# Optimization experiments

Measured on AMD Instinct MI355X. Metric: run time of the kernel, lower is better.

Reference implementation:

```python
import jax, jax.numpy as jnp
import numpy as np

B, S, E, NUM_CLASSES = 4, 4096, 256, 16

def setup_inputs() -> dict:
    key = jax.random.key(0)
    ks = jax.random.split(key, 10)
    std = E ** -0.5
    return {
        "x":  jax.random.normal(ks[0], (B, S, E), dtype=jnp.float32),
        "wq": jax.random.normal(ks[1], (E, E), dtype=jnp.float32) * std,
        "bq": jnp.zeros((E,), dtype=jnp.float32),
        "wk": jax.random.normal(ks[2], (E, E), dtype=jnp.float32) * std,
        "bk": jnp.zeros((E,), dtype=jnp.float32),
        "wv": jax.random.normal(ks[3], (E, E), dtype=jnp.float32) * std,
        "bv": jnp.zeros((E,), dtype=jnp.float32),
        "wo": jax.random.normal(ks[4], (NUM_CLASSES, E), dtype=jnp.float32) * std,
        "bo": jnp.zeros((NUM_CLASSES,), dtype=jnp.float32),
    }

def reference(x, wq, bq, wk, bk, wv, bv, wo, bo):
    embed_dim = wq.shape[0]
    scaling = embed_dim ** -0.5  # float(embed_dim) ** (-0.5)
    # torch Linear: y = x @ W.T + b
    Q = jnp.einsum('bse,oe->bso', x, wq) + bq
    K = jnp.einsum('bse,oe->bso', x, wk) + bk
    V = jnp.einsum('bse,oe->bso', x, wv) + bv
    # scores: [B, S, S]
    scores = jnp.einsum('bqe,bke->bqk', Q, K) * scaling
    # original code has `/ (embed_dim ^ 0.5)`; intended math is / sqrt(embed_dim)
    attn = jax.nn.softmax(scores, axis=-1) * scaling
    attn_out = jnp.einsum('bqk,bke->bqe', attn, V)
    return jnp.einsum('bqe,oe->bqo', attn_out, wo) + bo
```

## Files before the change

kernel.cpp:

```cpp
#include <hip/hip_runtime.h>
#include <hip/hip_bf16.h>


#define S_ 4096
#define E_ 256
#define B_ 4
#define NC_ 16
#define BS_ (B_ * S_)
#define NS_ 4

typedef __attribute__((ext_vector_type(8))) short bf16x8;
typedef __attribute__((ext_vector_type(4))) float f32x4;

__device__ __forceinline__ unsigned short bf16_rtne(float f) {
    unsigned int u = __float_as_uint(f);
    return (unsigned short)((u + 0x7FFFu + ((u >> 16) & 1u)) >> 16);
}
__device__ __forceinline__ bf16x8 pack8(f32x4 a, f32x4 b) {
    bf16x8 r;
#pragma unroll
    for (int i = 0; i < 4; i++) r[i] = (short)bf16_rtne(a[i]);
#pragma unroll
    for (int i = 0; i < 4; i++) r[4 + i] = (short)bf16_rtne(b[i]);
    return r;
}
__device__ __forceinline__ void gl_lds16(const void* g, void* lds) {
    __builtin_amdgcn_global_load_lds(
        (const __attribute__((address_space(1))) unsigned int*)g,
        (__attribute__((address_space(3))) unsigned int*)lds, 16, 0, 0);
}
__device__ __forceinline__ int swz_u(int q) { return q ^ ((q >> 3) & 7); }

#define XUNITS_ (BS_ * E_ / 8)
#define WUNITS_ (3 * E_ * E_ / 8)
#define WOUNITS_ (NC_ * E_ / 8)
#define ZUNITS_ (BS_ * NC_ / 8)
__global__ __launch_bounds__(256) void pack_xw(
    const float* __restrict__ x, const float* __restrict__ wq,
    const float* __restrict__ wk, const float* __restrict__ wv,
    const float* __restrict__ wo, short* __restrict__ xb,
    short* __restrict__ wb, short* __restrict__ wbo,
    float* __restrict__ partial) {
    int u = blockIdx.x * 256 + threadIdx.x;
    const float* src;
    short* dst;
    if (u < XUNITS_) {
        src = x + (size_t)u * 8;
        dst = xb + (size_t)u * 8;
    } else if (u < XUNITS_ + WUNITS_) {
        int u2 = u - XUNITS_;
        int sel = u2 >> 13;
        int off = (u2 & 8191) * 8;
        src = ((sel == 0) ? wq : (sel == 1) ? wk : wv) + off;
        dst = wb + sel * (E_ * E_) + off;
    } else if (u < XUNITS_ + WUNITS_ + WOUNITS_) {
        int u2 = u - (XUNITS_ + WUNITS_);
        src = wo + (size_t)u2 * 8;
        dst = wbo + (size_t)u2 * 8;
    } else {
        int zu = u - (XUNITS_ + WUNITS_ + WOUNITS_);
        f32x4 z = {0.f, 0.f, 0.f, 0.f};
        ((f32x4*)partial)[zu * 2] = z;
        ((f32x4*)partial)[zu * 2 + 1] = z;
        return;
    }
    f32x4 a = *(const f32x4*)src;
    f32x4 b = *(const f32x4*)(src + 4);
    *(bf16x8*)dst = pack8(a, b);
}

__global__ __launch_bounds__(256) void qkv_gemm(
    const short* __restrict__ xb, const short* __restrict__ wb,
    const float* __restrict__ bq, const float* __restrict__ bk,
    const float* __restrict__ bv, short* __restrict__ Qb,
    short* __restrict__ Kb, short* __restrict__ Vtc) {
    __shared__ __align__(16) short stg[2][10240];
    __shared__ __align__(16) short epi[16896];

    int t = threadIdx.x;
    int lin = blockIdx.x;
    int xcd = lin & 7, r8 = lin >> 3;
    int sel = r8 >> 5;
    int m0 = (((xcd << 5) | (r8 & 31))) * 64;
    int lane = t & 63, wid = t >> 6, quad = lane >> 4, idx = lane & 15;

    const short* wsel = wb + sel * (E_ * E_);
    const float* bias = (sel == 0) ? bq : (sel == 1) ? bk : bv;

    int ux = swz_u(t);
    const short* xsrc = xb + (size_t)(m0 + (ux >> 2)) * E_ + (ux & 3) * 8;
    const short* wsrc[4];
#pragma unroll
    for (int i = 0; i < 4; i++) {
        int q = i * 256 + t, u = swz_u(q);
        wsrc[i] = wsel + (size_t)(u >> 2) * E_ + (u & 3) * 8;
    }

    gl_lds16(xsrc, &stg[0][t * 8]);
#pragma unroll
    for (int i = 0; i < 4; i++) gl_lds16(wsrc[i], &stg[0][(256 + i * 256 + t) * 8]);

    f32x4 zf = {0.f, 0.f, 0.f, 0.f};
    f32x4 acc[16];
#pragma unroll
    for (int i = 0; i < 16; i++) acc[i] = zf;

    int fo = (idx * 4 + quad) ^ (idx >> 1);

    for (int it = 0; it < 8; it++) {
        __syncthreads();
        if (it < 7) {
            int kc = (it + 1) * 32;
            short* d = stg[(it + 1) & 1];
            gl_lds16(xsrc + kc, &d[t * 8]);
#pragma unroll
            for (int i = 0; i < 4; i++)
                gl_lds16(wsrc[i] + kc, &d[(256 + i * 256 + t) * 8]);
        }
        const short* cb = stg[it & 1];
        bf16x8 af = *(const bf16x8*)&cb[(wid * 64 + fo) * 8];
        const short* cw = &cb[(256 + fo) * 8];
        __builtin_amdgcn_s_setprio(1);
#pragma unroll
        for (int ct = 0; ct < 16; ct++)
            acc[ct] = __builtin_amdgcn_mfma_f32_16x16x32_bf16(
                af, *(const bf16x8*)&cw[ct * 512], acc[ct], 0, 0, 0);
        __builtin_amdgcn_s_setprio(0);
    }

    int qr = quad * 4;
    if (sel == 2) {
#pragma unroll
        for (int ct = 0; ct < 16; ct++) {
            int e = ct * 16 + idx;
            float bb = bias[e];
#pragma unroll
            for (int r = 0; r < 4; r++) {
                int mr = wid * 16 + qr + r;
                int ckg = mr >> 5, sin = mr & 31;
                int sp = ((sin & 15) << 1) | (sin >> 4);
                int pos = (sp >> 3) ^ ((e >> 1) & 3);
                epi[ckg * 8192 + e * 32 + pos * 8 + (sp & 7)] =
                    (short)bf16_rtne(acc[ct][r] + bb);
            }
        }
        __syncthreads();
        size_t base = ((size_t)((m0 >> 12) * 128 + ((m0 & (S_ - 1)) >> 5))) * 8192;
#pragma unroll
        for (int j = 0; j < 8; j++) {
            int unit = j * 256 + t;
            *(bf16x8*)(Vtc + base + (size_t)unit * 8) = *(const bf16x8*)&epi[unit * 8];
        }
    } else {
        float alpha = (sel == 0) ? 0.0625f : 1.0f;
#pragma unroll
        for (int ct = 0; ct < 16; ct++) {
            int n = ct * 16 + idx;
            float bb = bias[n];
#pragma unroll
            for (int r = 0; r < 4; r++) {
                int row = wid * 16 + qr + r;
                int col = (sel == 1) ? ((((n >> 3) ^ (row & 7)) << 3) | (n & 7)) : n;
                epi[row * 264 + col] = (short)bf16_rtne((acc[ct][r] + bb) * alpha);
            }
        }
        __syncthreads();
        short* out = (sel == 0) ? Qb : Kb;
#pragma unroll
        for (int j = 0; j < 8; j++) {
            int g = j * 256 + t;
            int row = g >> 5, seg = g & 31;
            *(bf16x8*)(out + (size_t)(m0 + row) * E_ + seg * 8) =
                *(const bf16x8*)&epi[row * 264 + seg * 8];
        }
    }
}

__global__ __launch_bounds__(256, 2) void flash_attn(
    const short* __restrict__ Qb, const short* __restrict__ Kb,
    const short* __restrict__ Vtc, const short* __restrict__ wbo,
    float* __restrict__ partial, float* __restrict__ lpart) {
    __shared__ __align__(16) short lds[37888];

    int t = threadIdx.x;
    int lin = blockIdx.x;
    int xcd = lin & 7, r8 = lin >> 3;
    int pair = (xcd << 1) | (r8 >> 5);
    int b = pair >> 2, slice = pair & 3, q0 = (r8 & 31) * 128;
    int key0 = slice * (S_ / NS_);
    const int nchunk = (S_ / NS_) / 32;
    int lane = t & 63, wv = t >> 6, quad = lane >> 4, idx = lane & 15;

    bf16x8 qf[2][8];
#pragma unroll
    for (int u = 0; u < 2; u++) {
        const short* qrow = Qb + (size_t)(b * S_ + q0 + u * 64 + wv * 16 + idx) * E_ + quad * 8;
#pragma unroll
        for (int c = 0; c < 8; c++) qf[u][c] = *(const bf16x8*)(qrow + c * 32);
    }

    f32x4 zf = {0.f, 0.f, 0.f, 0.f};
    f32x4 oacc[2][16];
#pragma unroll
    for (int u = 0; u < 2; u++)
#pragma unroll
        for (int i = 0; i < 16; i++) oacc[u][i] = zf;
    float ls[2][4] = {{0, 0, 0, 0}, {0, 0, 0, 0}};

    const short* kg = Kb + (size_t)(b * S_ + key0) * E_ + lane * 8;
    const short* vg = Vtc + ((size_t)(b * 128 + (key0 >> 5))) * 8192 + lane * 8;
    short* psw = lds + 32768 + wv * 1280;
    unsigned int* pswu = (unsigned int*)psw;
    int vsw = (quad ^ ((idx >> 1) & 3)) << 3;

#pragma unroll
    for (int j = 0; j < 4; j++) gl_lds16(kg + (wv * 4 + j) * 512, &lds[(wv * 4 + j) * 512]);
#pragma unroll
    for (int j = 0; j < 4; j++) gl_lds16(vg + (wv * 4 + j) * 512, &lds[16384 + (wv * 4 + j) * 512]);
#pragma unroll
    for (int j = 0; j < 4; j++) gl_lds16(kg + 8192 + (wv * 4 + j) * 512, &lds[8192 + (wv * 4 + j) * 512]);
    __syncthreads();

    {
        f32x4 s[4] = {zf, zf, zf, zf};
        __builtin_amdgcn_s_setprio(1);
#pragma unroll
        for (int c = 0; c < 8; c++) {
            int p = (((c * 4 + quad) ^ (idx & 7)) << 3);
            bf16x8 k0 = *(const bf16x8*)&lds[idx * 256 + p];
            bf16x8 k1 = *(const bf16x8*)&lds[(16 + idx) * 256 + p];
            s[0] = __builtin_amdgcn_mfma_f32_16x16x32_bf16(qf[0][c], k0, s[0], 0, 0, 0);
            s[1] = __builtin_amdgcn_mfma_f32_16x16x32_bf16(qf[0][c], k1, s[1], 0, 0, 0);
            s[2] = __builtin_amdgcn_mfma_f32_16x16x32_bf16(qf[1][c], k0, s[2], 0, 0, 0);
            s[3] = __builtin_amdgcn_mfma_f32_16x16x32_bf16(qf[1][c], k1, s[3], 0, 0, 0);
        }
        __builtin_amdgcn_s_setprio(0);
#pragma unroll
        for (int u = 0; u < 2; u++)
#pragma unroll
            for (int r = 0; r < 4; r++) {
                float p0 = __expf(s[u * 2][r]);
                float p1 = __expf(s[u * 2 + 1][r]);
                ls[u][r] += p0 + p1;
                pswu[u * 320 + (quad * 4 + r) * 20 + idx] =
                    (unsigned int)bf16_rtne(p0) | ((unsigned int)bf16_rtne(p1) << 16);
            }
    }

    for (int ck = 0; ck < nchunk - 1; ck++) {
        __syncthreads();
        bf16x8 af0 = *(const bf16x8*)&psw[idx * 40 + quad * 8];
        bf16x8 af1 = *(const bf16x8*)&psw[640 + idx * 40 + quad * 8];
        if (ck + 2 < nchunk) {
            const short* ks = kg + (size_t)(ck + 2) * 8192;
            short* kd = lds + (ck & 1) * 8192;
#pragma unroll
            for (int j = 0; j < 4; j++) gl_lds16(ks + (wv * 4 + j) * 512, &kd[(wv * 4 + j) * 512]);
        }
        {
            const short* vs = vg + (size_t)(ck + 1) * 8192;
            short* vd = lds + 16384 + ((ck + 1) & 1) * 8192;
#pragma unroll
            for (int j = 0; j < 4; j++) gl_lds16(vs + (wv * 4 + j) * 512, &vd[(wv * 4 + j) * 512]);
        }
        const short* kc = lds + ((ck + 1) & 1) * 8192;
        f32x4 s[4] = {zf, zf, zf, zf};
        __builtin_amdgcn_s_setprio(1);
#pragma unroll
        for (int c = 0; c < 8; c++) {
            int p = (((c * 4 + quad) ^ (idx & 7)) << 3);
            bf16x8 k0 = *(const bf16x8*)&kc[idx * 256 + p];
            bf16x8 k1 = *(const bf16x8*)&kc[(16 + idx) * 256 + p];
            s[0] = __builtin_amdgcn_mfma_f32_16x16x32_bf16(qf[0][c], k0, s[0], 0, 0, 0);
            s[1] = __builtin_amdgcn_mfma_f32_16x16x32_bf16(qf[0][c], k1, s[1], 0, 0, 0);
            s[2] = __builtin_amdgcn_mfma_f32_16x16x32_bf16(qf[1][c], k0, s[2], 0, 0, 0);
            s[3] = __builtin_amdgcn_mfma_f32_16x16x32_bf16(qf[1][c], k1, s[3], 0, 0, 0);
        }
        __builtin_amdgcn_s_setprio(0);
#pragma unroll
        for (int u = 0; u < 2; u++)
#pragma unroll
            for (int r = 0; r < 4; r++) {
                float p0 = __expf(s[u * 2][r]);
                float p1 = __expf(s[u * 2 + 1][r]);
                ls[u][r] += p0 + p1;
                pswu[u * 320 + (quad * 4 + r) * 20 + idx] =
                    (unsigned int)bf16_rtne(p0) | ((unsigned int)bf16_rtne(p1) << 16);
            }
        const short* vc = lds + 16384 + (ck & 1) * 8192;
        __builtin_amdgcn_s_setprio(1);
#pragma unroll
        for (int ct = 0; ct < 16; ct++) {
            bf16x8 v = *(const bf16x8*)&vc[(ct * 16 + idx) * 32 + vsw];
            oacc[0][ct] = __builtin_amdgcn_mfma_f32_16x16x32_bf16(af0, v, oacc[0][ct], 0, 0, 0);
            oacc[1][ct] = __builtin_amdgcn_mfma_f32_16x16x32_bf16(af1, v, oacc[1][ct], 0, 0, 0);
        }
        __builtin_amdgcn_s_setprio(0);
    }
    __syncthreads();
    {
        bf16x8 af0 = *(const bf16x8*)&psw[idx * 40 + quad * 8];
        bf16x8 af1 = *(const bf16x8*)&psw[640 + idx * 40 + quad * 8];
        const short* vc = lds + 16384 + ((nchunk - 1) & 1) * 8192;
        __builtin_amdgcn_s_setprio(1);
#pragma unroll
        for (int ct = 0; ct < 16; ct++) {
            bf16x8 v = *(const bf16x8*)&vc[(ct * 16 + idx) * 32 + vsw];
            oacc[0][ct] = __builtin_amdgcn_mfma_f32_16x16x32_bf16(af0, v, oacc[0][ct], 0, 0, 0);
            oacc[1][ct] = __builtin_amdgcn_mfma_f32_16x16x32_bf16(af1, v, oacc[1][ct], 0, 0, 0);
        }
        __builtin_amdgcn_s_setprio(0);
    }
    __syncthreads();

#pragma unroll
    for (int u = 0; u < 2; u++)
#pragma unroll
        for (int r = 0; r < 4; r++) {
            float v = ls[u][r];
            v += __shfl_xor(v, 1);
            v += __shfl_xor(v, 2);
            v += __shfl_xor(v, 4);
            v += __shfl_xor(v, 8);
            if (idx == 0)
                lpart[(size_t)slice * BS_ + b * S_ + q0 + u * 64 + wv * 16 + quad * 4 + r] = v;
        }

    short* scr = lds + wv * 8192;
#pragma unroll
    for (int u = 0; u < 2; u++)
#pragma unroll
        for (int ct = 0; ct < 16; ct++) {
            int e = ct * 16 + idx;
#pragma unroll
            for (int r = 0; r < 4; r++) {
                int lr = quad * 4 + r;
                scr[u * 4096 + lr * 256 + ((((e >> 3) ^ (lr & 7)) << 3) | (e & 7))] =
                    (short)bf16_rtne(oacc[u][ct][r]);
            }
        }

    f32x4 pacc[2] = {zf, zf};
#pragma unroll
    for (int c = 0; c < 8; c++) {
        bf16x8 bw = *(const bf16x8*)(wbo + idx * E_ + c * 32 + quad * 8);
#pragma unroll
        for (int u = 0; u < 2; u++) {
            bf16x8 af = *(const bf16x8*)&scr[u * 4096 + idx * 256 +
                                             (((c * 4 + quad) ^ (idx & 7)) << 3)];
            pacc[u] = __builtin_amdgcn_mfma_f32_16x16x32_bf16(af, bw, pacc[u], 0, 0, 0);
        }
    }
#pragma unroll
    for (int u = 0; u < 2; u++)
#pragma unroll
        for (int r = 0; r < 4; r++) {
            int m = q0 + u * 64 + wv * 16 + quad * 4 + r;
            atomicAdd(&partial[((size_t)b * S_ + m) * NC_ + idx], pacc[u][r]);
        }
}

__global__ __launch_bounds__(256) void norm_out(
    const float* __restrict__ partial, const float* __restrict__ lpart,
    const float* __restrict__ bo, float* __restrict__ out) {
    int t = threadIdx.x;
    int m = blockIdx.x * 16 + (t >> 4), o = t & 15;
    float ltot = 0.f;
#pragma unroll
    for (int ns = 0; ns < NS_; ns++) ltot += lpart[(size_t)ns * BS_ + m];
    size_t i = (size_t)m * NC_ + o;
    out[i] = partial[i] * (0.0625f / ltot) + bo[o];
}

extern "C" void kernel_launch(void* const* d_in, const int* in_sizes, int n_in,
                              void* d_out, int out_size, void* d_ws, size_t ws_size,
                              hipStream_t stream) {
    const float* x  = (const float*)d_in[0];
    const float* wq = (const float*)d_in[1];
    const float* bq = (const float*)d_in[2];
    const float* wk = (const float*)d_in[3];
    const float* bk = (const float*)d_in[4];
    const float* wv = (const float*)d_in[5];
    const float* bv = (const float*)d_in[6];
    const float* wo = (const float*)d_in[7];
    const float* bo = (const float*)d_in[8];
    float* out = (float*)d_out;

    const size_t NEL = (size_t)BS_ * E_;
    short* Qb = (short*)d_ws;
    short* Kb = Qb + NEL;
    short* Vtc = Kb + NEL;
    short* xb = Vtc + NEL;
    short* wb = xb + NEL;
    short* wbo = wb + (size_t)3 * E_ * E_;
    float* partial = (float*)(wbo + (size_t)NC_ * E_);
    float* lpart = partial + (size_t)BS_ * NC_;

    pack_xw<<<(XUNITS_ + WUNITS_ + WOUNITS_ + ZUNITS_) / 256, 256, 0, stream>>>(
        x, wq, wk, wv, wo, xb, wb, wbo, partial);
    qkv_gemm<<<dim3(768), 256, 0, stream>>>(xb, wb, bq, bk, bv, Qb, Kb, Vtc);
    flash_attn<<<dim3(512), 256, 0, stream>>>(Qb, Kb, Vtc, wbo, partial, lpart);
    norm_out<<<dim3(BS_ / 16), 256, 0, stream>>>(partial, lpart, bo, out);
}
```

Before: 170.3 us.

## Fuse x fp32-to-bf16 conversion into QKV GEMM A-fragment loads

The pack kernel no longer converts x to bf16. Instead, each QKV GEMM wave loads its fp32 x rows directly into registers, converts them to bf16 A fragments for all eight K steps up front, and streams only the weights through LDS. This removes the round trip of writing and re-reading the bf16 copy of x and shrinks the LDS staging buffer. The cost is that each x row is now read as fp32 three times, once per Q/K/V selector, and the kernel holds eight bf16x8 fragments per thread, which raises register pressure.

```diff
diff --git a/kernel.cpp b/kernel.cpp
--- a/kernel.cpp
+++ b/kernel.cpp
@@ -31,34 +31,28 @@
 }
 __device__ __forceinline__ int swz_u(int q) { return q ^ ((q >> 3) & 7); }
 
-#define XUNITS_ (BS_ * E_ / 8)
 #define WUNITS_ (3 * E_ * E_ / 8)
 #define WOUNITS_ (NC_ * E_ / 8)
 #define ZUNITS_ (BS_ * NC_ / 8)
-__global__ __launch_bounds__(256) void pack_xw(
-    const float* __restrict__ x, const float* __restrict__ wq,
-    const float* __restrict__ wk, const float* __restrict__ wv,
-    const float* __restrict__ wo, short* __restrict__ xb,
+__global__ __launch_bounds__(256) void pack_w(
+    const float* __restrict__ wq, const float* __restrict__ wk,
+    const float* __restrict__ wv, const float* __restrict__ wo,
     short* __restrict__ wb, short* __restrict__ wbo,
     float* __restrict__ partial) {
     int u = blockIdx.x * 256 + threadIdx.x;
     const float* src;
     short* dst;
-    if (u < XUNITS_) {
-        src = x + (size_t)u * 8;
-        dst = xb + (size_t)u * 8;
-    } else if (u < XUNITS_ + WUNITS_) {
-        int u2 = u - XUNITS_;
-        int sel = u2 >> 13;
-        int off = (u2 & 8191) * 8;
+    if (u < WUNITS_) {
+        int sel = u >> 13;
+        int off = (u & 8191) * 8;
         src = ((sel == 0) ? wq : (sel == 1) ? wk : wv) + off;
         dst = wb + sel * (E_ * E_) + off;
-    } else if (u < XUNITS_ + WUNITS_ + WOUNITS_) {
-        int u2 = u - (XUNITS_ + WUNITS_);
+    } else if (u < WUNITS_ + WOUNITS_) {
+        int u2 = u - WUNITS_;
         src = wo + (size_t)u2 * 8;
         dst = wbo + (size_t)u2 * 8;
     } else {
-        int zu = u - (XUNITS_ + WUNITS_ + WOUNITS_);
+        int zu = u - (WUNITS_ + WOUNITS_);
         f32x4 z = {0.f, 0.f, 0.f, 0.f};
         ((f32x4*)partial)[zu * 2] = z;
         ((f32x4*)partial)[zu * 2 + 1] = z;
@@ -70,11 +64,11 @@
 }
 
 __global__ __launch_bounds__(256) void qkv_gemm(
-    const short* __restrict__ xb, const short* __restrict__ wb,
+    const float* __restrict__ x, const short* __restrict__ wb,
     const float* __restrict__ bq, const float* __restrict__ bk,
     const float* __restrict__ bv, short* __restrict__ Qb,
     short* __restrict__ Kb, short* __restrict__ Vtc) {
-    __shared__ __align__(16) short stg[2][10240];
+    __shared__ __align__(16) short stg[2][8192];
     __shared__ __align__(16) short epi[16896];
 
     int t = threadIdx.x;
@@ -87,8 +81,6 @@
     const short* wsel = wb + sel * (E_ * E_);
     const float* bias = (sel == 0) ? bq : (sel == 1) ? bk : bv;
 
-    int ux = swz_u(t);
-    const short* xsrc = xb + (size_t)(m0 + (ux >> 2)) * E_ + (ux & 3) * 8;
     const short* wsrc[4];
 #pragma unroll
     for (int i = 0; i < 4; i++) {
@@ -96,9 +88,17 @@
         wsrc[i] = wsel + (size_t)(u >> 2) * E_ + (u & 3) * 8;
     }
 
-    gl_lds16(xsrc, &stg[0][t * 8]);
-#pragma unroll
-    for (int i = 0; i < 4; i++) gl_lds16(wsrc[i], &stg[0][(256 + i * 256 + t) * 8]);
+#pragma unroll
+    for (int i = 0; i < 4; i++) gl_lds16(wsrc[i], &stg[0][(i * 256 + t) * 8]);
+
+    const float* xrow = x + (size_t)(m0 + wid * 16 + idx) * E_ + quad * 8;
+    bf16x8 af[8];
+#pragma unroll
+    for (int it = 0; it < 8; it++) {
+        f32x4 a0 = *(const f32x4*)(xrow + it * 32);
+        f32x4 a1 = *(const f32x4*)(xrow + it * 32 + 4);
+        af[it] = pack8(a0, a1);
+    }
 
     f32x4 zf = {0.f, 0.f, 0.f, 0.f};
     f32x4 acc[16];
@@ -107,24 +107,22 @@
 
     int fo = (idx * 4 + quad) ^ (idx >> 1);
 
+#pragma unroll
     for (int it = 0; it < 8; it++) {
         __syncthreads();
         if (it < 7) {
             int kc = (it + 1) * 32;
             short* d = stg[(it + 1) & 1];
-            gl_lds16(xsrc + kc, &d[t * 8]);
 #pragma unroll
             for (int i = 0; i < 4; i++)
-                gl_lds16(wsrc[i] + kc, &d[(256 + i * 256 + t) * 8]);
-        }
-        const short* cb = stg[it & 1];
-        bf16x8 af = *(const bf16x8*)&cb[(wid * 64 + fo) * 8];
-        const short* cw = &cb[(256 + fo) * 8];
+                gl_lds16(wsrc[i] + kc, &d[(i * 256 + t) * 8]);
+        }
+        const short* cw = &stg[it & 1][fo * 8];
         __builtin_amdgcn_s_setprio(1);
 #pragma unroll
         for (int ct = 0; ct < 16; ct++)
             acc[ct] = __builtin_amdgcn_mfma_f32_16x16x32_bf16(
-                af, *(const bf16x8*)&cw[ct * 512], acc[ct], 0, 0, 0);
+                af[it], *(const bf16x8*)&cw[ct * 512], acc[ct], 0, 0, 0);
         __builtin_amdgcn_s_setprio(0);
     }
 
@@ -390,15 +388,14 @@
     short* Qb = (short*)d_ws;
     short* Kb = Qb + NEL;
     short* Vtc = Kb + NEL;
-    short* xb = Vtc + NEL;
-    short* wb = xb + NEL;
+    short* wb = Vtc + NEL;
     short* wbo = wb + (size_t)3 * E_ * E_;
     float* partial = (float*)(wbo + (size_t)NC_ * E_);
     float* lpart = partial + (size_t)BS_ * NC_;
 
-    pack_xw<<<(XUNITS_ + WUNITS_ + WOUNITS_ + ZUNITS_) / 256, 256, 0, stream>>>(
-        x, wq, wk, wv, wo, xb, wb, wbo, partial);
-    qkv_gemm<<<dim3(768), 256, 0, stream>>>(xb, wb, bq, bk, bv, Qb, Kb, Vtc);
+    pack_w<<<(WUNITS_ + WOUNITS_ + ZUNITS_) / 256, 256, 0, stream>>>(
+        wq, wk, wv, wo, wb, wbo, partial);
+    qkv_gemm<<<dim3(768), 256, 0, stream>>>(x, wb, bq, bk, bv, Qb, Kb, Vtc);
     flash_attn<<<dim3(512), 256, 0, stream>>>(Qb, Kb, Vtc, wbo, partial, lpart);
     norm_out<<<dim3(BS_ / 16), 256, 0, stream>>>(partial, lpart, bo, out);
 }
```

New measurement: 169.9 us. Within noise of the previous version (-0.2%).
